# Kernel optimization log

Hardware: AMD Instinct MI355X
Metric: run time of the kernel (lower is better)

## Reference

```python
import jax, jax.numpy as jnp
import numpy as np

WINDOW = 7
NUM_HEADS = 12

def _relative_position_index(ws: int) -> np.ndarray:
    coords = np.stack(np.meshgrid(np.arange(ws), np.arange(ws), indexing='ij'))  # (2, ws, ws)
    flat = coords.reshape(2, -1)  # (2, N)
    rel = flat[:, :, None] - flat[:, None, :]  # (2, N, N)
    rel = rel.transpose(1, 2, 0).copy()
    rel[:, :, 0] += ws - 1
    rel[:, :, 1] += ws - 1
    rel[:, :, 0] *= 2 * ws - 1
    return rel.sum(-1)  # (N, N) int

REL_IDX = jnp.asarray(_relative_position_index(WINDOW))  # (49, 49)

def setup_inputs() -> dict:
    key = jax.random.key(0)
    ks = jax.random.split(key, 7)
    B_, N, C = 2048, 49, 384
    nW = 64
    return {
        'x': jax.random.normal(ks[0], (B_, N, C), jnp.float32),
        'mask': jax.random.normal(ks[1], (nW, N, N), jnp.float32),
        'qkv_w': jax.random.normal(ks[2], (3 * C, C), jnp.float32) * 0.02,
        'qkv_b': jax.random.normal(ks[3], (3 * C,), jnp.float32) * 0.02,
        'proj_w': jax.random.normal(ks[4], (C, C), jnp.float32) * 0.02,
        'proj_b': jax.random.normal(ks[5], (C,), jnp.float32) * 0.02,
        'rel_bias_table': jax.random.normal(ks[6], ((2 * WINDOW - 1) ** 2, NUM_HEADS), jnp.float32) * 0.02,
    }

def reference(x, mask, qkv_w, qkv_b, proj_w, proj_b, rel_bias_table):
    B_, N, C = x.shape
    H = NUM_HEADS
    D = C // H
    scale = D ** -0.5
    # fused qkv projection: (B_, N, 3C) -> (3, B_, H, N, D)
    qkv = (x @ qkv_w.T + qkv_b).reshape(B_, N, 3, H, D).transpose(2, 0, 3, 1, 4)
    q, k, v = qkv[0], qkv[1], qkv[2]
    attn = jnp.einsum('bhnd,bhmd->bhnm', q, k) * scale  # (B_, H, N, N)
    # relative position bias gather: (N, N, H) -> (H, N, N)
    bias = rel_bias_table[REL_IDX].transpose(2, 0, 1)
    attn = attn + bias[None]
    nW = mask.shape[0]
    B = B_ // nW
    attn = attn.reshape(B, nW, H, N, N) + mask[None, :, None]
    attn = attn.reshape(B_, H, N, N)
    attn = jax.nn.softmax(attn, axis=-1)
    out = jnp.einsum('bhnm,bhmd->bnhd', attn, v).reshape(B_, N, C)
    return out @ proj_w.T + proj_b
```

## Files before the change

kernel.cpp:

```cpp
#include <hip/hip_runtime.h>
#include <hip/hip_bf16.h>
#include <stdint.h>
#include <stddef.h>

typedef __attribute__((ext_vector_type(8))) short short8;
typedef __attribute__((ext_vector_type(4))) float floatx4;

#define GLDS16(gptr, lptr)                                                         \
  __builtin_amdgcn_global_load_lds(                                                \
      (const __attribute__((address_space(1))) void*)(gptr),                       \
      (__attribute__((address_space(3))) void*)(lptr), 16, 0, 0)

#define MTOT  100352
#define KDIM  384
#define NQKV  1152
#define NPROJ 384

static __device__ __forceinline__ unsigned int bfu(float f) {
    __hip_bfloat16 h = __float2bfloat16(f);
    return (unsigned int)*(unsigned short*)&h;
}

__global__ void cvt_kernel(const float* __restrict__ in,
                           __hip_bfloat16* __restrict__ out, int n4) {
    int i = blockIdx.x * blockDim.x + threadIdx.x;
    if (i >= n4) return;
    float4 v = ((const float4*)in)[i];
    __hip_bfloat16* o = out + (size_t)i * 4;
    o[0] = __float2bfloat16(v.x);
    o[1] = __float2bfloat16(v.y);
    o[2] = __float2bfloat16(v.z);
    o[3] = __float2bfloat16(v.w);
}

__global__ void build_bias_kernel(const float* __restrict__ tbl,
                                  const float* __restrict__ mask,
                                  float* __restrict__ comb) {
    int tid = blockIdx.x * 256 + threadIdx.x;
    if (tid >= 12 * 64 * 49 * 52) return;
    int hw = tid / 2548;
    int nm = tid - hw * 2548;
    int row = nm / 52;
    int col = nm - row * 52;
    int h = hw >> 6;
    int w2 = hw & 63;
    float v = -1e30f;
    if (col < 49) {
        int i1 = row / 7, j1 = row - i1 * 7;
        int i2 = col / 7, j2 = col - i2 * 7;
        int ridx = (i1 - i2 + 6) * 13 + (j1 - j2 + 6);
        v = tbl[ridx * 12 + h] + mask[(size_t)w2 * 2401 + row * 49 + col];
    }
    comb[tid] = v;
}

template <int EPI>
__global__ __launch_bounds__(256, 4) void gemm_bt_kernel(
    const __hip_bfloat16* __restrict__ A, const __hip_bfloat16* __restrict__ B,
    const float* __restrict__ bias, float* __restrict__ Cout,
    __hip_bfloat16* __restrict__ Cbf, int N, int NBN) {
    __shared__ __hip_bfloat16 sA[128 * 64];
    __shared__ __hip_bfloat16 sB[128 * 64];
    const int t = threadIdx.x;
    const int per_chunk = 16 * NBN;
    const int chunk = blockIdx.x / per_chunk;
    const int rr = blockIdx.x - chunk * per_chunk;
    const int bn = rr >> 4;
    const int bm = chunk * 16 + (rr & 15);

    const int lane = t & 63;
    const int w = t >> 6;
    const int wm = w & 1, wn = w >> 1;
    const int quad = lane >> 4, l15 = lane & 15;
    const int srow = t >> 3;
    const int scg = t & 7;
    const int sg = scg ^ (srow & 7);
    const int rsw = l15 & 7;

    const __hip_bfloat16* Ab = A + (size_t)bm * 128 * KDIM;
    const __hip_bfloat16* Bb = B + (size_t)bn * 128 * KDIM;

    const floatx4 fzero = {0.f, 0.f, 0.f, 0.f};
    floatx4 acc[4][4];
#pragma unroll
    for (int i = 0; i < 4; ++i)
#pragma unroll
        for (int j = 0; j < 4; ++j) acc[i][j] = fzero;

    for (int kk = 0; kk < KDIM; kk += 64) {
#pragma unroll
        for (int i = 0; i < 4; ++i) {
            const int r0 = srow + i * 32;
            GLDS16(Ab + (size_t)r0 * KDIM + kk + sg * 8, &sA[r0 * 64 + scg * 8]);
            GLDS16(Bb + (size_t)r0 * KDIM + kk + sg * 8, &sB[r0 * 64 + scg * 8]);
        }
        __syncthreads();
#pragma unroll
        for (int kk2 = 0; kk2 < 2; ++kk2) {
            short8 af[4], bf[4];
#pragma unroll
            for (int i = 0; i < 4; ++i)
                af[i] = *(const short8*)&sA[(wm * 64 + i * 16 + l15) * 64 +
                                            ((kk2 * 4 + quad) ^ rsw) * 8];
#pragma unroll
            for (int j = 0; j < 4; ++j)
                bf[j] = *(const short8*)&sB[(wn * 64 + j * 16 + l15) * 64 +
                                            ((kk2 * 4 + quad) ^ rsw) * 8];
#pragma unroll
            for (int i = 0; i < 4; ++i)
#pragma unroll
                for (int j = 0; j < 4; ++j)
                    acc[i][j] = __builtin_amdgcn_mfma_f32_16x16x32_bf16(
                        bf[j], af[i], acc[i][j], 0, 0, 0);
        }
        __syncthreads();
    }

    if (EPI == 0) {
        const float scale = 0.17677669529663687f;
#pragma unroll
        for (int i = 0; i < 4; ++i) {
            const int m = bm * 128 + wm * 64 + i * 16 + l15;
#pragma unroll
            for (int j = 0; j < 4; ++j) {
                const int f0 = bn * 128 + wn * 64 + j * 16 + quad * 4;
                const float4 bv = *(const float4*)&bias[f0];
                const float sc = (f0 < 384) ? scale : 1.0f;
                uint2 pk;
                pk.x = bfu((acc[i][j][0] + bv.x) * sc) |
                       (bfu((acc[i][j][1] + bv.y) * sc) << 16);
                pk.y = bfu((acc[i][j][2] + bv.z) * sc) |
                       (bfu((acc[i][j][3] + bv.w) * sc) << 16);
                *(uint2*)&Cbf[(size_t)m * NQKV + f0] = pk;
            }
        }
    } else {
#pragma unroll
        for (int i = 0; i < 4; ++i) {
            const int m = bm * 128 + wm * 64 + i * 16 + l15;
#pragma unroll
            for (int j = 0; j < 4; ++j) {
                const int f0 = bn * 128 + wn * 64 + j * 16 + quad * 4;
                const float4 bv = *(const float4*)&bias[f0];
                float4 o;
                o.x = acc[i][j][0] + bv.x;
                o.y = acc[i][j][1] + bv.y;
                o.z = acc[i][j][2] + bv.z;
                o.w = acc[i][j][3] + bv.w;
                *(float4*)&Cout[(size_t)m * N + f0] = o;
            }
        }
    }
}

__global__ __launch_bounds__(64) void attn_kernel(
    const __hip_bfloat16* __restrict__ qkv,
    const float* __restrict__ comb,
    __hip_bfloat16* __restrict__ attn_out) {
    __shared__ unsigned short sP[64 * 72];
    __shared__ unsigned short sVB[4][66][8];
    const int id = blockIdx.x;
    const int h = id >> 11;
    const int rem = id & 2047;
    const int w = rem >> 5;
    const int b = rem & 31;
    const int b_ = b * 64 + w;
    const int lane = threadIdx.x;
    const int quad = lane >> 4, l15 = lane & 15;
    const short* base = (const short*)qkv + (size_t)b_ * 49 * 1152 + h * 32;

    const floatx4 fzero = {0.f, 0.f, 0.f, 0.f};

    short8 bQ[4], aK[4];
#pragma unroll
    for (int im = 0; im < 4; ++im) {
        int m = im * 16 + l15;
        m = m > 48 ? 48 : m;
        bQ[im] = *(const short8*)(base + (size_t)m * 1152 + quad * 8);
    }
#pragma unroll
    for (int jn = 0; jn < 4; ++jn) {
        int n = jn * 16 + l15;
        n = n > 48 ? 48 : n;
        aK[jn] = *(const short8*)(base + (size_t)n * 1152 + 384 + quad * 8);
    }
    const short8 zero8 = {0, 0, 0, 0, 0, 0, 0, 0};
#pragma unroll
    for (int jn = 0; jn < 4; ++jn) {
        const int n = jn * 16 + l15;
        const int nc = n > 48 ? 48 : n;
        short8 vv = *(const short8*)(base + (size_t)nc * 1152 + 768 + quad * 8);
        if (n > 48) vv = zero8;
        *(short8*)&sVB[quad][n][0] = vv;
    }

    floatx4 ST[4][4];
#pragma unroll
    for (int im = 0; im < 4; ++im)
#pragma unroll
        for (int jn = 0; jn < 4; ++jn)
            ST[im][jn] = __builtin_amdgcn_mfma_f32_16x16x32_bf16(aK[jn], bQ[im],
                                                                 fzero, 0, 0, 0);

    const float* cb = comb + (size_t)(h * 64 + w) * 2548;
#pragma unroll
    for (int im = 0; im < 4; ++im) {
        const int m = im * 16 + l15;
        const int mrow = m > 48 ? 48 : m;
        const float* rp = cb + mrow * 52;
        float v[16];
#pragma unroll
        for (int jn = 0; jn < 3; ++jn) {
            float4 c4 = *(const float4*)(rp + jn * 16 + quad * 4);
            v[jn * 4 + 0] = ST[im][jn][0] + c4.x;
            v[jn * 4 + 1] = ST[im][jn][1] + c4.y;
            v[jn * 4 + 2] = ST[im][jn][2] + c4.z;
            v[jn * 4 + 3] = ST[im][jn][3] + c4.w;
        }
        {
            const float s48 = rp[48];
            v[12] = (quad == 0) ? (ST[im][3][0] + s48) : -1e30f;
            v[13] = -1e30f;
            v[14] = -1e30f;
            v[15] = -1e30f;
        }
        float mx = v[0];
#pragma unroll
        for (int q = 1; q < 16; ++q) mx = fmaxf(mx, v[q]);
        mx = fmaxf(mx, __shfl_xor(mx, 16));
        mx = fmaxf(mx, __shfl_xor(mx, 32));
        float sum = 0.f;
#pragma unroll
        for (int q = 0; q < 16; ++q) {
            v[q] = __expf(v[q] - mx);
            sum += v[q];
        }
        sum += __shfl_xor(sum, 16);
        sum += __shfl_xor(sum, 32);
        const float inv = 1.0f / sum;
#pragma unroll
        for (int jn = 0; jn < 4; ++jn) {
            uint2 pk;
            pk.x = bfu(v[jn * 4 + 0] * inv) | (bfu(v[jn * 4 + 1] * inv) << 16);
            pk.y = bfu(v[jn * 4 + 2] * inv) | (bfu(v[jn * 4 + 3] * inv) << 16);
            *(uint2*)&sP[m * 72 + jn * 16 + quad * 4] = pk;
        }
    }
    __syncthreads();

    short8 aP[4][2];
#pragma unroll
    for (int im = 0; im < 4; ++im)
#pragma unroll
        for (int kk = 0; kk < 2; ++kk)
            aP[im][kk] =
                *(const short8*)&sP[(im * 16 + l15) * 72 + kk * 32 + quad * 8];

    short8 bV[2][2];
#pragma unroll
    for (int jd = 0; jd < 2; ++jd) {
        const int d = jd * 16 + l15;
        const int db = d >> 3, dl = d & 7;
#pragma unroll
        for (int kk = 0; kk < 2; ++kk) {
            short8 tmp;
#pragma unroll
            for (int jj = 0; jj < 8; ++jj)
                tmp[jj] = (short)sVB[db][kk * 32 + quad * 8 + jj][dl];
            bV[jd][kk] = tmp;
        }
    }

    floatx4 O[4][2];
#pragma unroll
    for (int im = 0; im < 4; ++im)
#pragma unroll
        for (int jd = 0; jd < 2; ++jd) {
            floatx4 o = __builtin_amdgcn_mfma_f32_16x16x32_bf16(bV[jd][0],
                                                                aP[im][0], fzero,
                                                                0, 0, 0);
            o = __builtin_amdgcn_mfma_f32_16x16x32_bf16(bV[jd][1], aP[im][1], o, 0,
                                                        0, 0);
            O[im][jd] = o;
        }

#pragma unroll
    for (int im = 0; im < 4; ++im) {
        const int m = im * 16 + l15;
        if (m < 49) {
#pragma unroll
            for (int jd = 0; jd < 2; ++jd) {
                uint2 pk;
                pk.x = bfu(O[im][jd][0]) | (bfu(O[im][jd][1]) << 16);
                pk.y = bfu(O[im][jd][2]) | (bfu(O[im][jd][3]) << 16);
                *(uint2*)&attn_out[((size_t)b_ * 49 + m) * 384 + h * 32 +
                                   jd * 16 + quad * 4] = pk;
            }
        }
    }
}

extern "C" void kernel_launch(void* const* d_in, const int* in_sizes, int n_in,
                              void* d_out, int out_size, void* d_ws,
                              size_t ws_size, hipStream_t stream) {
    (void)in_sizes; (void)n_in; (void)out_size; (void)ws_size;
    const float* x      = (const float*)d_in[0];
    const float* mask   = (const float*)d_in[1];
    const float* qkv_w  = (const float*)d_in[2];
    const float* qkv_b  = (const float*)d_in[3];
    const float* proj_w = (const float*)d_in[4];
    const float* proj_b = (const float*)d_in[5];
    const float* tbl    = (const float*)d_in[6];
    float* out = (float*)d_out;
    char* ws = (char*)d_ws;

    __hip_bfloat16* x_bf   = (__hip_bfloat16*)(ws);
    __hip_bfloat16* wq_bf  = (__hip_bfloat16*)(ws + 77070336);
    float*          comb   = (float*)(ws + 77070336);
    __hip_bfloat16* wp_bf  = (__hip_bfloat16*)(ws + 84897792);
    __hip_bfloat16* qkv_o  = (__hip_bfloat16*)(ws + 85192704);
    __hip_bfloat16* attn_o = x_bf;

    cvt_kernel<<<(MTOT * KDIM / 4 + 255) / 256, 256, 0, stream>>>(x, x_bf,
                                                                  MTOT * KDIM / 4);
    cvt_kernel<<<(NQKV * KDIM / 4 + 255) / 256, 256, 0, stream>>>(
        qkv_w, wq_bf, NQKV * KDIM / 4);
    cvt_kernel<<<(NPROJ * KDIM / 4 + 255) / 256, 256, 0, stream>>>(
        proj_w, wp_bf, NPROJ * KDIM / 4);
    gemm_bt_kernel<0><<<784 * 9, 256, 0, stream>>>(x_bf, wq_bf, qkv_b, nullptr,
                                                   qkv_o, NQKV, 9);
    build_bias_kernel<<<(12 * 64 * 49 * 52 + 255) / 256, 256, 0, stream>>>(
        tbl, mask, comb);
    attn_kernel<<<2048 * 12, 64, 0, stream>>>(qkv_o, comb, attn_o);
    gemm_bt_kernel<1><<<784 * 3, 256, 0, stream>>>(attn_o, wp_bf, proj_b, out,
                                                   nullptr, NPROJ, 3);
}
```

Before: 559.8 us.

## Triple-buffer GEMM K-loop with async LDS loads and 256x128 tiles

The bf16 GEMM now uses 512-thread blocks with 256x128 output tiles, and its LDS is triple-buffered. Global-to-LDS loads for k-step t+2 are issued while MFMAs run on step t, using manual vmcnt waits and raw barriers in place of __syncthreads. The intent is to hide global load latency behind MFMA work and to reuse the B tile across more rows. In exchange, LDS use per block grows to 144 KB and occupancy drops to one or two blocks per CU. The hand-written waitcnt counts also risk races if they are off.

```diff
diff --git a/kernel.cpp b/kernel.cpp
--- a/kernel.cpp
+++ b/kernel.cpp
@@ -54,30 +54,41 @@
     comb[tid] = v;
 }
 
+#define STAGE_HALF(T, H, BUF)                                                  \
+  do {                                                                         \
+    const size_t kb_ = (size_t)(T) * 64;                                       \
+    GLDS16(Ab + ((size_t)((H) * 128 + srow)) * KDIM + kb_ + sg * 8,            \
+           &sA[BUF][((H) * 128 + srow) * 64 + scg * 8]);                       \
+    GLDS16(Ab + ((size_t)((H) * 128 + 64 + srow)) * KDIM + kb_ + sg * 8,       \
+           &sA[BUF][((H) * 128 + 64 + srow) * 64 + scg * 8]);                  \
+    GLDS16(Bb + ((size_t)((H) * 64 + srow)) * KDIM + kb_ + sg * 8,             \
+           &sB[BUF][((H) * 64 + srow) * 64 + scg * 8]);                        \
+  } while (0)
+
 template <int EPI>
-__global__ __launch_bounds__(256, 4) void gemm_bt_kernel(
+__global__ __launch_bounds__(512, 2) void gemm_bt_kernel(
     const __hip_bfloat16* __restrict__ A, const __hip_bfloat16* __restrict__ B,
     const float* __restrict__ bias, float* __restrict__ Cout,
     __hip_bfloat16* __restrict__ Cbf, int N, int NBN) {
-    __shared__ __hip_bfloat16 sA[128 * 64];
-    __shared__ __hip_bfloat16 sB[128 * 64];
+    __shared__ __hip_bfloat16 sA[3][256 * 64];
+    __shared__ __hip_bfloat16 sB[3][128 * 64];
     const int t = threadIdx.x;
-    const int per_chunk = 16 * NBN;
+    const int per_chunk = 8 * NBN;
     const int chunk = blockIdx.x / per_chunk;
     const int rr = blockIdx.x - chunk * per_chunk;
-    const int bn = rr >> 4;
-    const int bm = chunk * 16 + (rr & 15);
+    const int bn = rr >> 3;
+    const int bm = chunk * 8 + (rr & 7);
 
     const int lane = t & 63;
     const int w = t >> 6;
-    const int wm = w & 1, wn = w >> 1;
+    const int wm = w & 3, wn = w >> 2;
     const int quad = lane >> 4, l15 = lane & 15;
     const int srow = t >> 3;
     const int scg = t & 7;
     const int sg = scg ^ (srow & 7);
     const int rsw = l15 & 7;
 
-    const __hip_bfloat16* Ab = A + (size_t)bm * 128 * KDIM;
+    const __hip_bfloat16* Ab = A + (size_t)bm * 256 * KDIM;
     const __hip_bfloat16* Bb = B + (size_t)bn * 128 * KDIM;
 
     const floatx4 fzero = {0.f, 0.f, 0.f, 0.f};
@@ -87,40 +98,54 @@
 #pragma unroll
         for (int j = 0; j < 4; ++j) acc[i][j] = fzero;
 
-    for (int kk = 0; kk < KDIM; kk += 64) {
-#pragma unroll
-        for (int i = 0; i < 4; ++i) {
-            const int r0 = srow + i * 32;
-            GLDS16(Ab + (size_t)r0 * KDIM + kk + sg * 8, &sA[r0 * 64 + scg * 8]);
-            GLDS16(Bb + (size_t)r0 * KDIM + kk + sg * 8, &sB[r0 * 64 + scg * 8]);
-        }
-        __syncthreads();
+    STAGE_HALF(0, 0, 0);
+    STAGE_HALF(0, 1, 0);
+    STAGE_HALF(1, 0, 1);
+    STAGE_HALF(1, 1, 1);
+    asm volatile("s_waitcnt vmcnt(6)" ::: "memory");
+    asm volatile("s_barrier" ::: "memory");
+
+#pragma unroll
+    for (int tt = 0; tt < 6; ++tt) {
+        const int bufc = tt % 3;
 #pragma unroll
         for (int kk2 = 0; kk2 < 2; ++kk2) {
             short8 af[4], bf[4];
+            const int cg = ((kk2 * 4 + quad) ^ rsw) * 8;
 #pragma unroll
             for (int i = 0; i < 4; ++i)
-                af[i] = *(const short8*)&sA[(wm * 64 + i * 16 + l15) * 64 +
-                                            ((kk2 * 4 + quad) ^ rsw) * 8];
+                af[i] = *(const short8*)&sA[bufc][(wm * 64 + i * 16 + l15) * 64 + cg];
 #pragma unroll
             for (int j = 0; j < 4; ++j)
-                bf[j] = *(const short8*)&sB[(wn * 64 + j * 16 + l15) * 64 +
-                                            ((kk2 * 4 + quad) ^ rsw) * 8];
+                bf[j] = *(const short8*)&sB[bufc][(wn * 64 + j * 16 + l15) * 64 + cg];
+            if (tt + 2 < 6) {
+                STAGE_HALF(tt + 2, kk2, (tt + 2) % 3);
+            }
+            asm volatile("s_barrier" ::: "memory");
+            __builtin_amdgcn_s_setprio(1);
 #pragma unroll
             for (int i = 0; i < 4; ++i)
 #pragma unroll
                 for (int j = 0; j < 4; ++j)
                     acc[i][j] = __builtin_amdgcn_mfma_f32_16x16x32_bf16(
                         bf[j], af[i], acc[i][j], 0, 0, 0);
-        }
-        __syncthreads();
+            __builtin_amdgcn_s_setprio(0);
+            if (kk2 == 1) {
+                if (tt + 2 < 6) {
+                    asm volatile("s_waitcnt vmcnt(6)" ::: "memory");
+                } else if (tt + 1 < 6) {
+                    asm volatile("s_waitcnt vmcnt(0)" ::: "memory");
+                }
+            }
+            asm volatile("s_barrier" ::: "memory");
+        }
     }
 
     if (EPI == 0) {
         const float scale = 0.17677669529663687f;
 #pragma unroll
         for (int i = 0; i < 4; ++i) {
-            const int m = bm * 128 + wm * 64 + i * 16 + l15;
+            const int m = bm * 256 + wm * 64 + i * 16 + l15;
 #pragma unroll
             for (int j = 0; j < 4; ++j) {
                 const int f0 = bn * 128 + wn * 64 + j * 16 + quad * 4;
@@ -137,7 +162,7 @@
     } else {
 #pragma unroll
         for (int i = 0; i < 4; ++i) {
-            const int m = bm * 128 + wm * 64 + i * 16 + l15;
+            const int m = bm * 256 + wm * 64 + i * 16 + l15;
 #pragma unroll
             for (int j = 0; j < 4; ++j) {
                 const int f0 = bn * 128 + wn * 64 + j * 16 + quad * 4;
@@ -327,11 +352,11 @@
         qkv_w, wq_bf, NQKV * KDIM / 4);
     cvt_kernel<<<(NPROJ * KDIM / 4 + 255) / 256, 256, 0, stream>>>(
         proj_w, wp_bf, NPROJ * KDIM / 4);
-    gemm_bt_kernel<0><<<784 * 9, 256, 0, stream>>>(x_bf, wq_bf, qkv_b, nullptr,
-                                                   qkv_o, NQKV, 9);
+    gemm_bt_kernel<0><<<49 * 8 * 9, 512, 0, stream>>>(x_bf, wq_bf, qkv_b,
+                                                      nullptr, qkv_o, NQKV, 9);
     build_bias_kernel<<<(12 * 64 * 49 * 52 + 255) / 256, 256, 0, stream>>>(
         tbl, mask, comb);
     attn_kernel<<<2048 * 12, 64, 0, stream>>>(qkv_o, comb, attn_o);
-    gemm_bt_kernel<1><<<784 * 3, 256, 0, stream>>>(attn_o, wp_bf, proj_b, out,
-                                                   nullptr, NPROJ, 3);
-}
+    gemm_bt_kernel<1><<<49 * 8 * 3, 512, 0, stream>>>(attn_o, wp_bf, proj_b,
+                                                      out, nullptr, NPROJ, 3);
+}
```

New measurement: 614.7 us. +9.8%, slower.

## Fuse fp32-to-bf16 input conversion into QKV GEMM tile loads

Applied to the files above, without the earlier changes.

Removes the standalone conversion pass over x. The QKV GEMM now loads fp32 tiles into shared memory with a swizzle and converts them to bf16 while building MFMA fragments. Both weight conversions are merged into a single launch. This avoids writing and re-reading a large bf16 copy of x, in exchange for doubled A-tile load bytes, more LDS, lower occupancy and extra conversion ALU work in the inner loop.

```diff
diff --git a/kernel.cpp b/kernel.cpp
--- a/kernel.cpp
+++ b/kernel.cpp
@@ -21,16 +21,24 @@
     return (unsigned int)*(unsigned short*)&h;
 }
 
-__global__ void cvt_kernel(const float* __restrict__ in,
-                           __hip_bfloat16* __restrict__ out, int n4) {
-    int i = blockIdx.x * blockDim.x + threadIdx.x;
-    if (i >= n4) return;
-    float4 v = ((const float4*)in)[i];
-    __hip_bfloat16* o = out + (size_t)i * 4;
-    o[0] = __float2bfloat16(v.x);
-    o[1] = __float2bfloat16(v.y);
-    o[2] = __float2bfloat16(v.z);
-    o[3] = __float2bfloat16(v.w);
+__global__ void cvt2_kernel(const float* __restrict__ wq,
+                            const float* __restrict__ wp,
+                            __hip_bfloat16* __restrict__ wqo,
+                            __hip_bfloat16* __restrict__ wpo) {
+    int i = blockIdx.x * 256 + threadIdx.x;
+    const float* src;
+    __hip_bfloat16* dst;
+    int j;
+    if (i < 110592) {
+        src = wq; dst = wqo; j = i;
+    } else {
+        src = wp; dst = wpo; j = i - 110592;
+    }
+    float4 v = ((const float4*)src)[j];
+    uint2 p;
+    p.x = bfu(v.x) | (bfu(v.y) << 16);
+    p.y = bfu(v.z) | (bfu(v.w) << 16);
+    *(uint2*)(dst + (size_t)j * 4) = p;
 }
 
 __global__ void build_bias_kernel(const float* __restrict__ tbl,
@@ -55,12 +63,16 @@
 }
 
 template <int EPI>
-__global__ __launch_bounds__(256, 4) void gemm_bt_kernel(
-    const __hip_bfloat16* __restrict__ A, const __hip_bfloat16* __restrict__ B,
-    const float* __restrict__ bias, float* __restrict__ Cout,
-    __hip_bfloat16* __restrict__ Cbf, int N, int NBN) {
-    __shared__ __hip_bfloat16 sA[128 * 64];
-    __shared__ __hip_bfloat16 sB[128 * 64];
+__global__ __launch_bounds__(256, EPI == 0 ? 3 : 4) void gemm_bt_kernel(
+    const float* __restrict__ Af32, const __hip_bfloat16* __restrict__ Abf,
+    const __hip_bfloat16* __restrict__ B, const float* __restrict__ bias,
+    float* __restrict__ Cout, __hip_bfloat16* __restrict__ Cbf, int N,
+    int NBN) {
+    __shared__ __align__(16) char smem[EPI == 0 ? 49152 : 32768];
+    __hip_bfloat16* sB = (__hip_bfloat16*)smem;
+    float* sAf = (float*)(smem + 16384);
+    __hip_bfloat16* sA = (__hip_bfloat16*)(smem + 16384);
+
     const int t = threadIdx.x;
     const int per_chunk = 16 * NBN;
     const int chunk = blockIdx.x / per_chunk;
@@ -76,8 +88,12 @@
     const int scg = t & 7;
     const int sg = scg ^ (srow & 7);
     const int rsw = l15 & 7;
-
-    const __hip_bfloat16* Ab = A + (size_t)bm * 128 * KDIM;
+    const int arow0 = t >> 4;
+    const int acg = t & 15;
+    const int asg = acg ^ arow0;
+
+    const float* Axb = Af32 + (size_t)bm * 128 * KDIM;
+    const __hip_bfloat16* Ab = Abf + (size_t)bm * 128 * KDIM;
     const __hip_bfloat16* Bb = B + (size_t)bn * 128 * KDIM;
 
     const floatx4 fzero = {0.f, 0.f, 0.f, 0.f};
@@ -88,20 +104,56 @@
         for (int j = 0; j < 4; ++j) acc[i][j] = fzero;
 
     for (int kk = 0; kk < KDIM; kk += 64) {
+        if (EPI == 0) {
+#pragma unroll
+            for (int i = 0; i < 8; ++i) {
+                const int r0 = arow0 + i * 16;
+                GLDS16(Axb + (size_t)r0 * KDIM + kk + asg * 4,
+                       &sAf[r0 * 64 + acg * 4]);
+            }
+        } else {
+#pragma unroll
+            for (int i = 0; i < 4; ++i) {
+                const int r0 = srow + i * 32;
+                GLDS16(Ab + (size_t)r0 * KDIM + kk + sg * 8,
+                       &sA[r0 * 64 + scg * 8]);
+            }
+        }
 #pragma unroll
         for (int i = 0; i < 4; ++i) {
             const int r0 = srow + i * 32;
-            GLDS16(Ab + (size_t)r0 * KDIM + kk + sg * 8, &sA[r0 * 64 + scg * 8]);
             GLDS16(Bb + (size_t)r0 * KDIM + kk + sg * 8, &sB[r0 * 64 + scg * 8]);
         }
         __syncthreads();
 #pragma unroll
         for (int kk2 = 0; kk2 < 2; ++kk2) {
             short8 af[4], bf[4];
-#pragma unroll
-            for (int i = 0; i < 4; ++i)
-                af[i] = *(const short8*)&sA[(wm * 64 + i * 16 + l15) * 64 +
-                                            ((kk2 * 4 + quad) ^ rsw) * 8];
+            if (EPI == 0) {
+#pragma unroll
+                for (int i = 0; i < 4; ++i) {
+                    const int arow = wm * 64 + i * 16 + l15;
+                    const int c0 = kk2 * 8 + quad * 2;
+                    const float4 fa =
+                        *(const float4*)&sAf[arow * 64 + (c0 ^ l15) * 4];
+                    const float4 fb =
+                        *(const float4*)&sAf[arow * 64 + ((c0 + 1) ^ l15) * 4];
+                    short8 a;
+                    a[0] = (short)bfu(fa.x);
+                    a[1] = (short)bfu(fa.y);
+                    a[2] = (short)bfu(fa.z);
+                    a[3] = (short)bfu(fa.w);
+                    a[4] = (short)bfu(fb.x);
+                    a[5] = (short)bfu(fb.y);
+                    a[6] = (short)bfu(fb.z);
+                    a[7] = (short)bfu(fb.w);
+                    af[i] = a;
+                }
+            } else {
+#pragma unroll
+                for (int i = 0; i < 4; ++i)
+                    af[i] = *(const short8*)&sA[(wm * 64 + i * 16 + l15) * 64 +
+                                                ((kk2 * 4 + quad) ^ rsw) * 8];
+            }
 #pragma unroll
             for (int j = 0; j < 4; ++j)
                 bf[j] = *(const short8*)&sB[(wn * 64 + j * 16 + l15) * 64 +
@@ -314,24 +366,19 @@
     float* out = (float*)d_out;
     char* ws = (char*)d_ws;
 
-    __hip_bfloat16* x_bf   = (__hip_bfloat16*)(ws);
     __hip_bfloat16* wq_bf  = (__hip_bfloat16*)(ws + 77070336);
     float*          comb   = (float*)(ws + 77070336);
     __hip_bfloat16* wp_bf  = (__hip_bfloat16*)(ws + 84897792);
     __hip_bfloat16* qkv_o  = (__hip_bfloat16*)(ws + 85192704);
-    __hip_bfloat16* attn_o = x_bf;
-
-    cvt_kernel<<<(MTOT * KDIM / 4 + 255) / 256, 256, 0, stream>>>(x, x_bf,
-                                                                  MTOT * KDIM / 4);
-    cvt_kernel<<<(NQKV * KDIM / 4 + 255) / 256, 256, 0, stream>>>(
-        qkv_w, wq_bf, NQKV * KDIM / 4);
-    cvt_kernel<<<(NPROJ * KDIM / 4 + 255) / 256, 256, 0, stream>>>(
-        proj_w, wp_bf, NPROJ * KDIM / 4);
-    gemm_bt_kernel<0><<<784 * 9, 256, 0, stream>>>(x_bf, wq_bf, qkv_b, nullptr,
-                                                   qkv_o, NQKV, 9);
+    __hip_bfloat16* attn_o = (__hip_bfloat16*)(ws);
+
+    cvt2_kernel<<<576, 256, 0, stream>>>(qkv_w, proj_w, wq_bf, wp_bf);
+    gemm_bt_kernel<0><<<784 * 9, 256, 0, stream>>>(x, nullptr, wq_bf, qkv_b,
+                                                   nullptr, qkv_o, NQKV, 9);
     build_bias_kernel<<<(12 * 64 * 49 * 52 + 255) / 256, 256, 0, stream>>>(
         tbl, mask, comb);
     attn_kernel<<<2048 * 12, 64, 0, stream>>>(qkv_o, comb, attn_o);
-    gemm_bt_kernel<1><<<784 * 3, 256, 0, stream>>>(attn_o, wp_bf, proj_b, out,
-                                                   nullptr, NPROJ, 3);
-}
+    gemm_bt_kernel<1><<<784 * 3, 256, 0, stream>>>(nullptr, attn_o, wp_bf,
+                                                   proj_b, out, nullptr, NPROJ,
+                                                   3);
+}
```

New measurement: 568.0 us. Within noise of the previous version (+1.5%).
